# Kernel optimization log

Hardware: AMD Instinct MI355X
Metric: run time of the kernel (lower is better)

Reference implementation:

```python
import jax, jax.numpy as jnp
import numpy as np
from jax import lax

B, C_IN, N, C_OUT, K = 16, 128, 2048, 256, 20
EPS = 1e-5


def setup_inputs() -> dict:
    key = jax.random.key(0)
    k1, k2 = jax.random.split(key)
    x = jax.random.normal(k1, (B, C_IN, N), dtype=jnp.float32)
    W = jax.random.normal(k2, (C_OUT, 2 * C_IN), dtype=jnp.float32) * (1.0 / np.sqrt(2 * C_IN))
    gamma = jnp.ones((C_OUT,), dtype=jnp.float32)
    beta = jnp.zeros((C_OUT,), dtype=jnp.float32)
    return {"x": x, "W": W, "gamma": gamma, "beta": beta, "k": K}


def _knn_inds(x, k):
    # squared pairwise distance: (B, N, N); computed with no grad (stop_gradient)
    xs = lax.stop_gradient(x)
    inner = jnp.einsum('bcn,bcm->bnm', xs, xs)
    sq = jnp.sum(xs * xs, axis=1)  # (B, N)
    pd = sq[:, :, None] - 2.0 * inner + sq[:, None, :]
    _, inds = lax.top_k(-pd, k)  # smallest distances -> (B, N, k)
    return inds


def reference(x, W, gamma, beta, k):
    knn = _knn_inds(x, k)                                   # (B, N, k) int
    # gather neighbours: neigh[b,c,n,j] = x[b,c,knn[b,n,j]]
    neigh = jax.vmap(lambda xb, kb: xb[:, kb])(x, knn)      # (B, C, N, k)
    central = jnp.broadcast_to(x[:, :, :, None], neigh.shape)
    edge = jnp.concatenate([central, neigh - central], axis=1)  # (B, 2C, N, k)
    # 1x1 conv (bias-free) as GEMM
    y = jnp.einsum('oc,bcnk->bonk', W, edge)                # (B, C_out, N, k)
    # BatchNorm2d (training-mode batch stats) + affine
    mean = jnp.mean(y, axis=(0, 2, 3), keepdims=True)
    var = jnp.var(y, axis=(0, 2, 3), keepdims=True)
    y = (y - mean) * lax.rsqrt(var + EPS)
    y = y * gamma[None, :, None, None] + beta[None, :, None, None]
    y = jax.nn.relu(y)
    return jnp.max(y, axis=3)                               # (B, C_out, N)
```

## Files before the change

### kernel.cpp

```cpp
#include <hip/hip_runtime.h>

#define B_   16
#define CIN  128
#define NPT  2048
#define COUT 256
#define KNN  20
#define KEEP 16
#define SIFT 32
#define EPS  1e-5f
#define DBIAS 256.0f

#define SQ_OFF   0ull
#define IDX_OFF  131072ull
#define UT_OFF   2752512ull
#define VT_OFF   36306944ull
#define GS_OFF   69861376ull
#define ST_OFF   69865472ull
#define AMAX_OFF 69871616ull
#define AMIN_OFF 103426048ull
#define WS_NEED_FUSED 136980480ull
#define XT_OFF   UT_OFF
#define XHT_OFF  VT_OFF

typedef _Float16 f16x8 __attribute__((ext_vector_type(8)));
typedef _Float16 f16x4 __attribute__((ext_vector_type(4)));
typedef float    f32x4 __attribute__((ext_vector_type(4)));
typedef float    f32x2 __attribute__((ext_vector_type(2)));

__global__ __launch_bounds__(256) void prep_kernel(const float* __restrict__ x,
                                                   const float* __restrict__ W,
                                                   float* __restrict__ xT,
                                                   _Float16* __restrict__ xhT,
                                                   _Float16* __restrict__ Wu,
                                                   _Float16* __restrict__ Wv,
                                                   float* __restrict__ sqh) {
    __shared__ float Ls[128 * 68];
    __shared__ float ps[4 * 64];
    const int id  = blockIdx.x;
    const int xcd = id & 7, qq = id >> 3;
    const int b   = xcd + ((qq >> 5) << 3);
    const int n0  = (qq & 31) * 64;
    const int t = threadIdx.x;
    if (Wu != nullptr && id < 128) {
        int gid = id * 256 + t;
        int o = gid >> 7, c = gid & 127;
        float w1 = W[o * 256 + c], w2 = W[o * 256 + 128 + c];
        Wu[gid] = (_Float16)(w1 - w2);
        Wv[gid] = (_Float16)w2;
    }
    const float* xb = x + (size_t)b * CIN * NPT;
    #pragma unroll
    for (int e = 0; e < 8; ++e) {
        int f = e * 256 + t;
        int c = f >> 4, n4 = (f & 15) << 2;
        *(float4*)&Ls[c * 68 + n4] = *(const float4*)&xb[(size_t)c * NPT + n0 + n4];
    }
    __syncthreads();
    {
        int nl = t & 63, part = t >> 6;
        float acc = 0.f;
        #pragma unroll
        for (int j = 0; j < 32; ++j) {
            float vh = (float)(_Float16)Ls[(part * 32 + j) * 68 + nl];
            acc += vh * vh;
        }
        ps[part * 64 + nl] = acc;
    }
    #pragma unroll
    for (int e = 0; e < 2; ++e) {
        int u = e * 256 + t;
        int nl = u >> 3, ck = (u & 7) << 4;
        float vv[16];
        #pragma unroll
        for (int j = 0; j < 16; ++j) vv[j] = Ls[(ck + j) * 68 + nl];
        size_t row = (size_t)b * NPT + n0 + nl;
        #pragma unroll
        for (int j = 0; j < 4; ++j) {
            float4 w = {vv[4 * j], vv[4 * j + 1], vv[4 * j + 2], vv[4 * j + 3]};
            *(float4*)&xT[row * CIN + ck + 4 * j] = w;
        }
        f16x8 h0, h1;
        #pragma unroll
        for (int j = 0; j < 8; ++j) { h0[j] = (_Float16)vv[j]; h1[j] = (_Float16)vv[8 + j]; }
        *(f16x8*)&xhT[row * CIN + ck] = h0;
        *(f16x8*)&xhT[row * CIN + ck + 8] = h1;
    }
    __syncthreads();
    if (t < 64) sqh[b * NPT + n0 + t] = ps[t] + ps[64 + t] + ps[128 + t] + ps[192 + t];
}

__device__ __forceinline__ void stage_pts(const _Float16* __restrict__ xhb,
                                          _Float16* buf, int base_n, int t) {
    const int l15 = t & 15, ks = t >> 6;
    const int quad = (t >> 4) & 3;
    const int c = ks * 32 + quad * 8;
    #pragma unroll
    for (int e = 0; e < 4; ++e) {
        const int n = base_n + e * 16 + l15;
        const _Float16* src = xhb + (size_t)n * CIN + c;
        _Float16* dst = buf + (size_t)(e * 256 + (t & 192)) * 8;
        __builtin_amdgcn_global_load_lds(
            (const __attribute__((address_space(1))) void*)src,
            (__attribute__((address_space(3))) void*)dst, 16, 0, 0);
    }
}

__device__ __forceinline__ void stage_tile16(const _Float16* __restrict__ srcl,
                                             _Float16* dsthalf) {
    #pragma unroll
    for (int e = 0; e < 4; ++e) {
        __builtin_amdgcn_global_load_lds(
            (const __attribute__((address_space(1))) void*)(srcl + e * 32),
            (__attribute__((address_space(3))) void*)(dsthalf + (size_t)e * 512),
            16, 0, 0);
    }
}

__global__ __launch_bounds__(256, 2) void knn_kernel(const _Float16* __restrict__ xhT,
                                                     const float* __restrict__ sqh,
                                                     int* __restrict__ surv_out) {
    __shared__ char smraw[59392];
    _Float16* bufA = (_Float16*)smraw;
    float*    sqm  = (float*)(smraw + 18432);

    const int id  = blockIdx.x;
    const int xcd = id & 7, qq = id >> 3;
    const int b   = xcd + ((qq >> 5) << 3);
    const int q0  = (qq & 31) * 64;
    const int t  = threadIdx.x;
    const int lane = t & 63, wv = t >> 6;
    const int l15 = lane & 15, quad = lane >> 4;
    const _Float16* xhb = xhT + (size_t)b * NPT * CIN;

    #pragma unroll
    for (int e = 0; e < 8; ++e)
        sqm[e * 256 + t] = sqh[b * NPT + e * 256 + t] + DBIAS;

    stage_pts(xhb, bufA, q0, t);
    __syncthreads();

    f16x8 af[4][4];
    #pragma unroll
    for (int qh = 0; qh < 4; ++qh)
        #pragma unroll
        for (int ks = 0; ks < 4; ++ks)
            af[qh][ks] = *(const f16x8*)(bufA + (size_t)((qh * 4 + ks) * 64 + lane) * 8);
    __syncthreads();

    _Float16* wbuf = (_Float16*)(smraw + 26624 + wv * 8192);
    float*    DtW  = (float*)(smraw + wv * 4608);
    const _Float16* srcl = xhb + (size_t)(wv * 16 + l15) * CIN + quad * 8;

    stage_tile16(srcl, wbuf);

    float bd[KEEP];
    #pragma unroll
    for (int i = 0; i < KEEP; ++i) bd[i] = 3.0e38f;

    #pragma unroll 1
    for (int ss = 0; ss < 32; ++ss) {
        const int mb = ss * 64 + wv * 16;
        asm volatile("s_waitcnt vmcnt(0)" ::: "memory");
        __builtin_amdgcn_sched_barrier(0);
        const _Float16* cur = wbuf + (ss & 1) * 2048;
        f16x8 bf[4];
        #pragma unroll
        for (int ks = 0; ks < 4; ++ks)
            bf[ks] = *(const f16x8*)(cur + ks * 512 + lane * 8);
        float sm_ = sqm[mb + l15];
        asm volatile("s_waitcnt lgkmcnt(0)" ::: "memory");
        __builtin_amdgcn_sched_barrier(0);
        if (ss < 31)
            stage_tile16(srcl + (size_t)(ss + 1) * 64 * CIN,
                         wbuf + ((ss + 1) & 1) * 2048);
        __builtin_amdgcn_sched_barrier(0);
        f32x4 acc[4];
        #pragma unroll
        for (int qh = 0; qh < 4; ++qh) acc[qh] = (f32x4){0.f, 0.f, 0.f, 0.f};
        #pragma unroll
        for (int ks = 0; ks < 4; ++ks)
            #pragma unroll
            for (int qh = 0; qh < 4; ++qh)
                acc[qh] = __builtin_amdgcn_mfma_f32_16x16x32_f16(af[qh][ks], bf[ks], acc[qh], 0, 0, 0);
        const unsigned om = (unsigned)(mb + l15);
        #pragma unroll
        for (int qh = 0; qh < 4; ++qh) {
            #pragma unroll
            for (int rg = 0; rg < 4; ++rg) {
                int q = qh * 16 + quad * 4 + rg;
                float d = sm_ - 2.f * acc[qh][rg];
                DtW[q * 18 + l15] = __uint_as_float((__float_as_uint(d) & 0xFFFFF800u) | om);
            }
        }
        float nk[16];
        {
            const float* myrow = DtW + lane * 18;
            #pragma unroll
            for (int p = 0; p < 8; ++p) {
                f32x2 v = *(const f32x2*)(myrow + 2 * p);
                nk[2 * p] = v[0]; nk[2 * p + 1] = v[1];
            }
        }
        #pragma unroll
        for (int kk = 2; kk <= 16; kk <<= 1) {
            #pragma unroll
            for (int j = kk >> 1; j > 0; j >>= 1) {
                #pragma unroll
                for (int i = 0; i < 16; ++i) {
                    int p = i ^ j;
                    if (p > i) {
                        float a = nk[i], c = nk[p];
                        float lo = fminf(a, c), hi = fmaxf(a, c);
                        if ((i & kk) == 0) { nk[i] = lo; nk[p] = hi; }
                        else               { nk[i] = hi; nk[p] = lo; }
                    }
                }
            }
        }
        #pragma unroll
        for (int i = 0; i < 16; ++i) bd[i] = fminf(bd[i], nk[15 - i]);
        #pragma unroll
        for (int j = 8; j > 0; j >>= 1) {
            #pragma unroll
            for (int i = 0; i < 16; ++i) {
                int p = i ^ j;
                if (p > i) {
                    float a = bd[i], c = bd[p];
                    bd[i] = fminf(a, c);
                    bd[p] = fmaxf(a, c);
                }
            }
        }
    }

    __syncthreads();

    float* Keys = (float*)smraw;
    #pragma unroll
    for (int i = 0; i < KEEP; ++i)
        Keys[lane * 65 + wv * KEEP + i] = bd[i];
    __syncthreads();
    {
        int cnt[KEEP];
        #pragma unroll
        for (int i = 0; i < KEEP; ++i) cnt[i] = 0;
        #pragma unroll 4
        for (int j = 0; j < 64; ++j) {
            float kj = Keys[lane * 65 + j];
            #pragma unroll
            for (int i = 0; i < KEEP; ++i)
                cnt[i] += (kj < bd[i]) ? 1 : 0;
        }
        int* dst = surv_out + ((size_t)b * NPT + q0 + lane) * SIFT;
        #pragma unroll
        for (int i = 0; i < KEEP; ++i)
            if (cnt[i] < SIFT)
                dst[cnt[i]] = (int)(__float_as_uint(bd[i]) & 0x7FFu);
    }
}

__global__ __launch_bounds__(256, 4) void refine_kernel(const float* __restrict__ xT,
                                                        const int* __restrict__ surv,
                                                        int* __restrict__ knn_out) {
    __shared__ float  Qs[16 * 128];
    __shared__ int    sidx[16 * 32];
    __shared__ double ddL[16 * 32];
    const int id  = blockIdx.x;
    const int xcd = id & 7, qq = id >> 3;
    const int b   = xcd + ((qq >> 7) << 3);
    const int q0  = (qq & 127) * 16;
    const int t = threadIdx.x;
    const float* xTb = xT + (size_t)b * NPT * CIN;
    #pragma unroll
    for (int e = 0; e < 2; ++e)
        sidx[e * 256 + t] = surv[((size_t)b * NPT + q0) * SIFT + e * 256 + t];
    #pragma unroll
    for (int e = 0; e < 2; ++e) {
        int f = e * 256 + t;
        int row = f >> 5, c4 = (f & 31) << 2;
        *(float4*)&Qs[row * 128 + c4] = *(const float4*)&xTb[(size_t)(q0 + row) * CIN + c4];
    }
    __syncthreads();
    const int g = t >> 3, j = t & 7;
    #pragma unroll 1
    for (int it = 0; it < 16; ++it) {
        int pair = it * 32 + g;
        int q = pair >> 5, k = pair & 31;
        int m = sidx[q * 32 + k];
        const float* mrow = xTb + (size_t)m * CIN + j * 16;
        const float* qrow = Qs + q * 128 + j * 16;
        float4 a0 = *(const float4*)&mrow[0];
        float4 a1 = *(const float4*)&mrow[4];
        float4 a2 = *(const float4*)&mrow[8];
        float4 a3 = *(const float4*)&mrow[12];
        float4 c0 = *(const float4*)&qrow[0];
        float4 c1 = *(const float4*)&qrow[4];
        float4 c2 = *(const float4*)&qrow[8];
        float4 c3 = *(const float4*)&qrow[12];
        double ss = 0.0, d0;
        d0 = (double)c0.x - (double)a0.x; ss = fma(d0, d0, ss);
        d0 = (double)c0.y - (double)a0.y; ss = fma(d0, d0, ss);
        d0 = (double)c0.z - (double)a0.z; ss = fma(d0, d0, ss);
        d0 = (double)c0.w - (double)a0.w; ss = fma(d0, d0, ss);
        d0 = (double)c1.x - (double)a1.x; ss = fma(d0, d0, ss);
        d0 = (double)c1.y - (double)a1.y; ss = fma(d0, d0, ss);
        d0 = (double)c1.z - (double)a1.z; ss = fma(d0, d0, ss);
        d0 = (double)c1.w - (double)a1.w; ss = fma(d0, d0, ss);
        d0 = (double)c2.x - (double)a2.x; ss = fma(d0, d0, ss);
        d0 = (double)c2.y - (double)a2.y; ss = fma(d0, d0, ss);
        d0 = (double)c2.z - (double)a2.z; ss = fma(d0, d0, ss);
        d0 = (double)c2.w - (double)a2.w; ss = fma(d0, d0, ss);
        d0 = (double)c3.x - (double)a3.x; ss = fma(d0, d0, ss);
        d0 = (double)c3.y - (double)a3.y; ss = fma(d0, d0, ss);
        d0 = (double)c3.z - (double)a3.z; ss = fma(d0, d0, ss);
        d0 = (double)c3.w - (double)a3.w; ss = fma(d0, d0, ss);
        ss += __shfl_xor(ss, 1, 8);
        ss += __shfl_xor(ss, 2, 8);
        ss += __shfl_xor(ss, 4, 8);
        if (j == 0) ddL[q * 32 + k] = ss;
    }
    __syncthreads();
    const int q = t >> 4, kk = (t & 15) << 1;
    int* dst = knn_out + ((size_t)b * NPT + q0 + q) * KNN;
    #pragma unroll
    for (int e = 0; e < 2; ++e) {
        int k = kk + e;
        double mine = ddL[q * 32 + k];
        int c = 0;
        #pragma unroll 4
        for (int jx = 0; jx < SIFT; ++jx)
            c += (ddL[q * 32 + jx] < mine) ? 1 : 0;
        if (c < KNN) dst[c] = sidx[q * 32 + k];
    }
}

__global__ __launch_bounds__(256, 2) void knn_kernel_fb(const _Float16* __restrict__ xhT,
                                                        const float* __restrict__ xT,
                                                        const float* __restrict__ sqh,
                                                        int* __restrict__ knn_out) {
    __shared__ char smraw[59392];
    _Float16* bufA = (_Float16*)smraw;
    float*    sqm  = (float*)(smraw + 18432);

    const int b  = blockIdx.y;
    const int q0 = blockIdx.x * 64;
    const int t  = threadIdx.x;
    const int lane = t & 63, wv = t >> 6;
    const int l15 = lane & 15, quad = lane >> 4;
    const _Float16* xhb = xhT + (size_t)b * NPT * CIN;

    #pragma unroll
    for (int e = 0; e < 8; ++e)
        sqm[e * 256 + t] = sqh[b * NPT + e * 256 + t] + DBIAS;

    stage_pts(xhb, bufA, q0, t);
    __syncthreads();

    f16x8 af[4][4];
    #pragma unroll
    for (int qh = 0; qh < 4; ++qh)
        #pragma unroll
        for (int ks = 0; ks < 4; ++ks)
            af[qh][ks] = *(const f16x8*)(bufA + (size_t)((qh * 4 + ks) * 64 + lane) * 8);
    __syncthreads();

    _Float16* wbuf = (_Float16*)(smraw + 26624 + wv * 8192);
    float*    DtW  = (float*)(smraw + wv * 4608);
    const _Float16* srcl = xhb + (size_t)(wv * 16 + l15) * CIN + quad * 8;
    stage_tile16(srcl, wbuf);

    float bd[KEEP];
    #pragma unroll
    for (int i = 0; i < KEEP; ++i) bd[i] = 3.0e38f;

    #pragma unroll 1
    for (int ss = 0; ss < 32; ++ss) {
        const int mb = ss * 64 + wv * 16;
        asm volatile("s_waitcnt vmcnt(0)" ::: "memory");
        __builtin_amdgcn_sched_barrier(0);
        const _Float16* cur = wbuf + (ss & 1) * 2048;
        f16x8 bf[4];
        #pragma unroll
        for (int ks = 0; ks < 4; ++ks)
            bf[ks] = *(const f16x8*)(cur + ks * 512 + lane * 8);
        float sm_ = sqm[mb + l15];
        asm volatile("s_waitcnt lgkmcnt(0)" ::: "memory");
        __builtin_amdgcn_sched_barrier(0);
        if (ss < 31)
            stage_tile16(srcl + (size_t)(ss + 1) * 64 * CIN,
                         wbuf + ((ss + 1) & 1) * 2048);
        __builtin_amdgcn_sched_barrier(0);
        f32x4 acc[4];
        #pragma unroll
        for (int qh = 0; qh < 4; ++qh) acc[qh] = (f32x4){0.f, 0.f, 0.f, 0.f};
        #pragma unroll
        for (int ks = 0; ks < 4; ++ks)
            #pragma unroll
            for (int qh = 0; qh < 4; ++qh)
                acc[qh] = __builtin_amdgcn_mfma_f32_16x16x32_f16(af[qh][ks], bf[ks], acc[qh], 0, 0, 0);
        const unsigned om = (unsigned)(mb + l15);
        #pragma unroll
        for (int qh = 0; qh < 4; ++qh) {
            #pragma unroll
            for (int rg = 0; rg < 4; ++rg) {
                int q = qh * 16 + quad * 4 + rg;
                float d = sm_ - 2.f * acc[qh][rg];
                DtW[q * 18 + l15] = __uint_as_float((__float_as_uint(d) & 0xFFFFF800u) | om);
            }
        }
        float nk[16];
        {
            const float* myrow = DtW + lane * 18;
            #pragma unroll
            for (int p = 0; p < 8; ++p) {
                f32x2 v = *(const f32x2*)(myrow + 2 * p);
                nk[2 * p] = v[0]; nk[2 * p + 1] = v[1];
            }
        }
        #pragma unroll
        for (int kk = 2; kk <= 16; kk <<= 1) {
            #pragma unroll
            for (int j = kk >> 1; j > 0; j >>= 1) {
                #pragma unroll
                for (int i = 0; i < 16; ++i) {
                    int p = i ^ j;
                    if (p > i) {
                        float a = nk[i], c = nk[p];
                        float lo = fminf(a, c), hi = fmaxf(a, c);
                        if ((i & kk) == 0) { nk[i] = lo; nk[p] = hi; }
                        else               { nk[i] = hi; nk[p] = lo; }
                    }
                }
            }
        }
        #pragma unroll
        for (int i = 0; i < 16; ++i) bd[i] = fminf(bd[i], nk[15 - i]);
        #pragma unroll
        for (int j = 8; j > 0; j >>= 1) {
            #pragma unroll
            for (int i = 0; i < 16; ++i) {
                int p = i ^ j;
                if (p > i) {
                    float a = bd[i], c = bd[p];
                    bd[i] = fminf(a, c);
                    bd[p] = fmaxf(a, c);
                }
            }
        }
    }

    __syncthreads();

    float*  Keys = (float*)smraw;
    int*    Surv = (int*)(smraw + 16640);
    double* ddL  = (double*)(smraw + 25088);
    #pragma unroll
    for (int i = 0; i < KEEP; ++i)
        Keys[lane * 65 + wv * KEEP + i] = bd[i];
    __syncthreads();
    {
        int cnt[KEEP];
        #pragma unroll
        for (int i = 0; i < KEEP; ++i) cnt[i] = 0;
        #pragma unroll 4
        for (int j = 0; j < 64; ++j) {
            float kj = Keys[lane * 65 + j];
            #pragma unroll
            for (int i = 0; i < KEEP; ++i)
                cnt[i] += (kj < bd[i]) ? 1 : 0;
        }
        __syncthreads();
        #pragma unroll
        for (int i = 0; i < KEEP; ++i)
            if (cnt[i] < SIFT)
                Surv[lane * 33 + cnt[i]] = (int)(__float_as_uint(bd[i]) & 0x7FFu);
    }
    __syncthreads();

    int ms[8];
    #pragma unroll
    for (int k = 0; k < 8; ++k) ms[k] = Surv[lane * 33 + wv * 8 + k] & 2047;
    double dd8[8];
    #pragma unroll
    for (int k = 0; k < 8; ++k) dd8[k] = 0.0;
    const float* xTb = xT + (size_t)b * NPT * CIN;
    const float* qrow = xTb + (size_t)(q0 + lane) * CIN;
    #pragma unroll 1
    for (int ch = 0; ch < 8; ++ch) {
        double qd[16];
        #pragma unroll
        for (int j = 0; j < 4; ++j) {
            float4 qv = *(const float4*)&qrow[ch * 16 + 4 * j];
            qd[4 * j] = (double)qv.x; qd[4 * j + 1] = (double)qv.y;
            qd[4 * j + 2] = (double)qv.z; qd[4 * j + 3] = (double)qv.w;
        }
        #pragma unroll
        for (int k = 0; k < 8; ++k) {
            const float* mrow = xTb + (size_t)ms[k] * CIN + ch * 16;
            float4 ma = *(const float4*)&mrow[0];
            float4 mb2 = *(const float4*)&mrow[4];
            float4 mc = *(const float4*)&mrow[8];
            float4 md = *(const float4*)&mrow[12];
            double ss = dd8[k], d0;
            d0 = qd[0]  - (double)ma.x;  ss = fma(d0, d0, ss);
            d0 = qd[1]  - (double)ma.y;  ss = fma(d0, d0, ss);
            d0 = qd[2]  - (double)ma.z;  ss = fma(d0, d0, ss);
            d0 = qd[3]  - (double)ma.w;  ss = fma(d0, d0, ss);
            d0 = qd[4]  - (double)mb2.x; ss = fma(d0, d0, ss);
            d0 = qd[5]  - (double)mb2.y; ss = fma(d0, d0, ss);
            d0 = qd[6]  - (double)mb2.z; ss = fma(d0, d0, ss);
            d0 = qd[7]  - (double)mb2.w; ss = fma(d0, d0, ss);
            d0 = qd[8]  - (double)mc.x;  ss = fma(d0, d0, ss);
            d0 = qd[9]  - (double)mc.y;  ss = fma(d0, d0, ss);
            d0 = qd[10] - (double)mc.z;  ss = fma(d0, d0, ss);
            d0 = qd[11] - (double)mc.w;  ss = fma(d0, d0, ss);
            d0 = qd[12] - (double)md.x;  ss = fma(d0, d0, ss);
            d0 = qd[13] - (double)md.y;  ss = fma(d0, d0, ss);
            d0 = qd[14] - (double)md.z;  ss = fma(d0, d0, ss);
            d0 = qd[15] - (double)md.w;  ss = fma(d0, d0, ss);
            dd8[k] = ss;
        }
    }
    #pragma unroll
    for (int k = 0; k < 8; ++k) ddL[lane * 33 + wv * 8 + k] = dd8[k];
    __syncthreads();
    int* dst = knn_out + ((size_t)b * NPT + q0 + lane) * KNN;
    #pragma unroll
    for (int k = 0; k < 8; ++k) {
        int c = 0;
        #pragma unroll 4
        for (int j = 0; j < SIFT; ++j)
            c += (ddL[lane * 33 + j] < dd8[k]) ? 1 : 0;
        if (c < KNN) dst[c] = ms[k];
    }
}

__global__ __launch_bounds__(256) void uv_gemm_h(const _Float16* __restrict__ xhT,
                                                 const _Float16* __restrict__ Wu,
                                                 const _Float16* __restrict__ Wv,
                                                 _Float16* __restrict__ uT,
                                                 _Float16* __restrict__ vT) {
    __shared__ _Float16 Bx[8192];
    const int id  = blockIdx.x;
    const int xcd = id & 7, qq = id >> 3;
    const int b   = xcd + ((qq >> 5) << 3);
    const int n0  = (qq & 31) * 64;
    const int t = threadIdx.x;
    const int lane = t & 63, w = t >> 6, l15 = lane & 15, quad = lane >> 4;
    stage_pts(xhT + (size_t)b * NPT * CIN, Bx, n0, t);
    __syncthreads();
    f16x8 bf[4];
    #pragma unroll
    for (int ks = 0; ks < 4; ++ks)
        bf[ks] = *(const f16x8*)(Bx + (size_t)((w * 4 + ks) * 64 + lane) * 8);
    const int n = n0 + w * 16 + l15;
    #pragma unroll 1
    for (int ot = 0; ot < 16; ++ot) {
        const _Float16* wu = Wu + (size_t)(ot * 16 + l15) * 128 + quad * 8;
        const _Float16* wv2 = Wv + (size_t)(ot * 16 + l15) * 128 + quad * 8;
        f32x4 au = (f32x4){0.f, 0.f, 0.f, 0.f};
        f32x4 av = (f32x4){0.f, 0.f, 0.f, 0.f};
        #pragma unroll
        for (int ks = 0; ks < 4; ++ks) {
            f16x8 a_u = *(const f16x8*)(wu + ks * 32);
            f16x8 a_v = *(const f16x8*)(wv2 + ks * 32);
            au = __builtin_amdgcn_mfma_f32_16x16x32_f16(a_u, bf[ks], au, 0, 0, 0);
            av = __builtin_amdgcn_mfma_f32_16x16x32_f16(a_v, bf[ks], av, 0, 0, 0);
        }
        size_t base = ((size_t)b * NPT + n) * COUT + ot * 16 + quad * 4;
        f16x4 auh = {(_Float16)au[0], (_Float16)au[1], (_Float16)au[2], (_Float16)au[3]};
        f16x4 avh = {(_Float16)av[0], (_Float16)av[1], (_Float16)av[2], (_Float16)av[3]};
        *(f16x4*)&uT[base] = auh;
        *(f16x4*)&vT[base] = avh;
    }
}

__global__ __launch_bounds__(256) void uv_gemm(const float* __restrict__ x,
                                               const float* __restrict__ W,
                                               float* __restrict__ uT,
                                               float* __restrict__ vT) {
    __shared__ float Ax[32 * 64];
    __shared__ float Bu[32 * 68];
    __shared__ float Bv[32 * 68];
    const int b  = blockIdx.z;
    const int n0 = blockIdx.x * 64;
    const int o0 = blockIdx.y * 64;
    const int t  = threadIdx.x;
    const int tx = t & 15, ty = t >> 4;
    const float* xb = x + (size_t)b * CIN * NPT;
    float au[4][4], av_[4][4];
    #pragma unroll
    for (int i = 0; i < 4; ++i)
        #pragma unroll
        for (int j = 0; j < 4; ++j) { au[i][j] = 0.f; av_[i][j] = 0.f; }
    #pragma unroll 1
    for (int kc = 0; kc < 4; ++kc) {
        const int c0 = kc * 32;
        __syncthreads();
        #pragma unroll
        for (int e = 0; e < 2; ++e) {
            int f = e * 256 + t;
            int cz = f >> 4, ni = (f & 15) << 2;
            *(float4*)&Ax[(cz << 6) + ni] = *(const float4*)&xb[(size_t)(c0 + cz) * NPT + n0 + ni];
        }
        #pragma unroll
        for (int e = 0; e < 8; ++e) {
            int ii = e * 256 + t;
            int cz = ii & 31, oj = ii >> 5;
            float w1 = W[(size_t)(o0 + oj) * 256 + c0 + cz];
            float w2 = W[(size_t)(o0 + oj) * 256 + 128 + c0 + cz];
            Bu[cz * 68 + oj] = w1 - w2;
            Bv[cz * 68 + oj] = w2;
        }
        __syncthreads();
        #pragma unroll 8
        for (int cz = 0; cz < 32; ++cz) {
            const float4 a4 = *(const float4*)&Ax[(cz << 6) + (tx << 2)];
            float bu0 = Bu[cz * 68 + (ty << 2) + 0], bv0 = Bv[cz * 68 + (ty << 2) + 0];
            float bu1 = Bu[cz * 68 + (ty << 2) + 1], bv1 = Bv[cz * 68 + (ty << 2) + 1];
            float bu2 = Bu[cz * 68 + (ty << 2) + 2], bv2 = Bv[cz * 68 + (ty << 2) + 2];
            float bu3 = Bu[cz * 68 + (ty << 2) + 3], bv3 = Bv[cz * 68 + (ty << 2) + 3];
            au[0][0] += a4.x * bu0; au[0][1] += a4.x * bu1; au[0][2] += a4.x * bu2; au[0][3] += a4.x * bu3;
            au[1][0] += a4.y * bu0; au[1][1] += a4.y * bu1; au[1][2] += a4.y * bu2; au[1][3] += a4.y * bu3;
            au[2][0] += a4.z * bu0; au[2][1] += a4.z * bu1; au[2][2] += a4.z * bu2; au[2][3] += a4.z * bu3;
            au[3][0] += a4.w * bu0; au[3][1] += a4.w * bu1; au[3][2] += a4.w * bu2; au[3][3] += a4.w * bu3;
            av_[0][0] += a4.x * bv0; av_[0][1] += a4.x * bv1; av_[0][2] += a4.x * bv2; av_[0][3] += a4.x * bv3;
            av_[1][0] += a4.y * bv0; av_[1][1] += a4.y * bv1; av_[1][2] += a4.y * bv2; av_[1][3] += a4.y * bv3;
            av_[2][0] += a4.z * bv0; av_[2][1] += a4.z * bv1; av_[2][2] += a4.z * bv2; av_[2][3] += a4.z * bv3;
            av_[3][0] += a4.w * bv0; av_[3][1] += a4.w * bv1; av_[3][2] += a4.w * bv2; av_[3][3] += a4.w * bv3;
        }
    }
    #pragma unroll
    for (int i = 0; i < 4; ++i) {
        int n = n0 + (tx << 2) + i;
        size_t base = ((size_t)b * NPT + n) * COUT + o0 + (ty << 2);
        float4 u4 = {au[i][0], au[i][1], au[i][2], au[i][3]};
        float4 v4 = {av_[i][0], av_[i][1], av_[i][2], av_[i][3]};
        *(float4*)&uT[base] = u4;
        *(float4*)&vT[base] = v4;
    }
}

__global__ __launch_bounds__(256) void gather_stats(const _Float16* __restrict__ uT,
                                                    const _Float16* __restrict__ vT,
                                                    const int* __restrict__ knn_in,
                                                    double* __restrict__ gsum,
                                                    _Float16* __restrict__ aMax,
                                                    _Float16* __restrict__ aMin) {
    __shared__ int sidx[16 * KNN];
    const int id  = blockIdx.x;
    const int xcd = id & 7, qq = id >> 3;
    const int b   = xcd + ((qq >> 7) << 3);
    const int inner = qq & 127;
    const int n0  = (inner >> 2) * 64 + (inner & 3) * 16;
    const int o   = threadIdx.x;
    for (int e = o; e < 16 * KNN; e += 256)
        sidx[e] = knn_in[((size_t)b * NPT + n0) * KNN + e];
    __syncthreads();
    const _Float16* ub = uT + ((size_t)b * NPT + n0) * COUT + o;
    const _Float16* vb = vT + (size_t)b * NPT * COUT + o;
    _Float16* amx = aMax + ((size_t)b * NPT + n0) * COUT + o;
    _Float16* amn = aMin + ((size_t)b * NPT + n0) * COUT + o;
    double s1 = 0.0, s2 = 0.0;
    #pragma unroll 1
    for (int s = 0; s < 16; ++s) {
        float u = (float)ub[(size_t)s * COUT];
        float vmax = -3e38f, vmin = 3e38f, vsum = 0.f, vsq = 0.f;
        #pragma unroll
        for (int j = 0; j < KNN; ++j) {
            float v = (float)vb[(size_t)sidx[s * KNN + j] * COUT];
            vmax = fmaxf(vmax, v);
            vmin = fminf(vmin, v);
            vsum += v;
            vsq = fmaf(v, v, vsq);
        }
        s1 += 20.0 * (double)u + (double)vsum;
        s2 += 20.0 * (double)u * (double)u + 2.0 * (double)u * (double)vsum + (double)vsq;
        _Float16 y1 = (_Float16)(u + vmax);
        _Float16 y2 = (_Float16)(u + vmin);
        __builtin_nontemporal_store(y1, &amx[(size_t)s * COUT]);
        __builtin_nontemporal_store(y2, &amn[(size_t)s * COUT]);
    }
    atomicAdd(&gsum[o], s1);
    atomicAdd(&gsum[COUT + o], s2);
}

__global__ __launch_bounds__(256) void stats_kernel(const float* __restrict__ uT,
                                                    const float* __restrict__ vT,
                                                    const int* __restrict__ knn_in,
                                                    double* __restrict__ gsum) {
    __shared__ int sidx[64 * KNN];
    const int b  = blockIdx.y;
    const int n0 = blockIdx.x * 64;
    const int o  = threadIdx.x;
    for (int e = o; e < 64 * KNN; e += 256)
        sidx[e] = knn_in[((size_t)b * NPT + n0) * KNN + e];
    __syncthreads();
    const float* ub = uT + ((size_t)b * NPT + n0) * COUT + o;
    const float* vb = vT + (size_t)b * NPT * COUT + o;
    double s1 = 0.0, s2 = 0.0;
    #pragma unroll 1
    for (int s = 0; s < 64; ++s) {
        float u = ub[(size_t)s * COUT];
        #pragma unroll
        for (int j = 0; j < KNN; ++j) {
            float y = u + vb[(size_t)sidx[s * KNN + j] * COUT];
            s1 += (double)y;
            s2 = fma((double)y, (double)y, s2);
        }
    }
    atomicAdd(&gsum[o], s1);
    atomicAdd(&gsum[COUT + o], s2);
}

__global__ void finalize_kernel(const double* __restrict__ gsum,
                                const float* __restrict__ gamma,
                                const float* __restrict__ beta,
                                float* __restrict__ st) {
    const int o = threadIdx.x;
    const double M = (double)B_ * NPT * KNN;
    double mean = gsum[o] / M;
    double var  = gsum[COUT + o] / M - mean * mean;
    float inv = 1.0f / sqrtf((float)var + EPS);
    float s = gamma[o] * inv;
    st[o] = s;
    st[COUT + o] = beta[o] - (float)mean * s;
}

__global__ __launch_bounds__(256, 2) void out2_kernel(const _Float16* __restrict__ aMax,
                                                      const _Float16* __restrict__ aMin,
                                                      const double* __restrict__ gsum,
                                                      const float* __restrict__ gamma,
                                                      const float* __restrict__ beta,
                                                      float* __restrict__ out) {
    __shared__ float zt[256 * 68];
    const int id  = blockIdx.x;
    const int xcd = id & 7, qq = id >> 3;
    const int b   = xcd + ((qq >> 5) << 3);
    const int n0  = (qq & 31) * 64;
    const int o = threadIdx.x;
    const double M = (double)B_ * NPT * KNN;
    double mean = gsum[o] / M;
    double var  = gsum[COUT + o] / M - mean * mean;
    float inv = 1.0f / sqrtf((float)var + EPS);
    const float s  = gamma[o] * inv;
    const float tt = beta[o] - (float)mean * s;
    const _Float16* amx = aMax + ((size_t)b * NPT + n0) * COUT + o;
    const _Float16* amn = aMin + ((size_t)b * NPT + n0) * COUT + o;
    #pragma unroll 2
    for (int si = 0; si < 64; ++si) {
        float y1 = (float)amx[(size_t)si * COUT];
        float y2 = (float)amn[(size_t)si * COUT];
        float z1 = fmaxf(s * y1 + tt, 0.f);
        float z2 = fmaxf(s * y2 + tt, 0.f);
        zt[o * 68 + si] = fmaxf(z1, z2);
    }
    __syncthreads();
    float* dst = out + ((size_t)b * COUT + o) * NPT + n0;
    #pragma unroll
    for (int i = 0; i < 16; ++i)
        *(float4*)&dst[i * 4] = *(const float4*)&zt[o * 68 + i * 4];
}

__global__ __launch_bounds__(256, 2) void out_kernel(const float* __restrict__ uT,
                                                     const float* __restrict__ vT,
                                                     const int* __restrict__ knn_in,
                                                     const float* __restrict__ st,
                                                     float* __restrict__ out) {
    __shared__ int sidx[64 * KNN];
    __shared__ float zt[256 * 68];
    const int b  = blockIdx.y;
    const int n0 = blockIdx.x * 64;
    const int o  = threadIdx.x;
    for (int e = o; e < 64 * KNN; e += 256)
        sidx[e] = knn_in[((size_t)b * NPT + n0) * KNN + e];
    __syncthreads();
    const float s  = st[o];
    const float tt = st[COUT + o];
    const float* ub = uT + ((size_t)b * NPT + n0) * COUT + o;
    const float* vb = vT + (size_t)b * NPT * COUT + o;
    #pragma unroll 1
    for (int si = 0; si < 64; ++si) {
        float u = ub[(size_t)si * COUT];
        float ymax = -3e38f, ymin = 3e38f;
        #pragma unroll
        for (int j = 0; j < KNN; ++j) {
            float y = u + vb[(size_t)sidx[si * KNN + j] * COUT];
            ymax = fmaxf(ymax, y);
            ymin = fminf(ymin, y);
        }
        float z1 = fmaxf(s * ymax + tt, 0.f);
        float z2 = fmaxf(s * ymin + tt, 0.f);
        zt[o * 68 + si] = fmaxf(z1, z2);
    }
    __syncthreads();
    float* dst = out + ((size_t)b * COUT + o) * NPT + n0;
    #pragma unroll
    for (int i = 0; i < 16; ++i)
        *(float4*)&dst[i * 4] = *(const float4*)&zt[o * 68 + i * 4];
}

extern "C" void kernel_launch(void* const* d_in, const int* in_sizes, int n_in,
                              void* d_out, int out_size, void* d_ws, size_t ws_size,
                              hipStream_t stream) {
    const float* x     = (const float*)d_in[0];
    const float* W     = (const float*)d_in[1];
    const float* gamma = (const float*)d_in[2];
    const float* beta  = (const float*)d_in[3];
    float* out = (float*)d_out;
    char* ws = (char*)d_ws;
    float*     sqh  = (float*)(ws + SQ_OFF);
    int*       idx  = (int*)(ws + IDX_OFF);
    double*    gsum = (double*)(ws + GS_OFF);
    float*     st   = (float*)(ws + ST_OFF);
    const bool fused = (ws_size >= WS_NEED_FUSED);

    hipMemsetAsync(gsum, 0, 2 * COUT * sizeof(double), stream);
    if (fused) {
        float*    xT   = (float*)(ws + AMAX_OFF);
        _Float16* xhT  = (_Float16*)(ws + AMAX_OFF + 16777216ull);
        _Float16* Wu   = (_Float16*)(ws + AMAX_OFF + 25165824ull);
        _Float16* Wv   = (_Float16*)(ws + AMAX_OFF + 25231360ull);
        int*      svG  = (int*)(ws + UT_OFF);
        _Float16* uTh  = (_Float16*)(ws + UT_OFF);
        _Float16* vTh  = (_Float16*)(ws + VT_OFF);
        _Float16* aMxh = (_Float16*)(ws + AMAX_OFF);
        _Float16* aMnh = (_Float16*)(ws + AMIN_OFF);
        prep_kernel<<<512, 256, 0, stream>>>(x, W, xT, xhT, Wu, Wv, sqh);
        knn_kernel<<<512, 256, 0, stream>>>(xhT, sqh, svG);
        refine_kernel<<<2048, 256, 0, stream>>>(xT, svG, idx);
        uv_gemm_h<<<512, 256, 0, stream>>>(xhT, Wu, Wv, uTh, vTh);
        gather_stats<<<2048, 256, 0, stream>>>(uTh, vTh, idx, gsum, aMxh, aMnh);
        out2_kernel<<<512, 256, 0, stream>>>(aMxh, aMnh, gsum, gamma, beta, out);
    } else {
        float*    xT  = (float*)(ws + XT_OFF);
        _Float16* xhT = (_Float16*)(ws + XHT_OFF);
        float*    uT  = (float*)(ws + UT_OFF);
        float*    vT  = (float*)(ws + VT_OFF);
        prep_kernel<<<512, 256, 0, stream>>>(x, W, xT, xhT, nullptr, nullptr, sqh);
        knn_kernel_fb<<<dim3(32, 16), 256, 0, stream>>>(xhT, xT, sqh, idx);
        uv_gemm<<<dim3(32, 4, 16), 256, 0, stream>>>(x, W, uT, vT);
        stats_kernel<<<dim3(32, 16), 256, 0, stream>>>(uT, vT, idx, gsum);
        finalize_kernel<<<1, 256, 0, stream>>>(gsum, gamma, beta, st);
        out_kernel<<<dim3(32, 16), 256, 0, stream>>>(uT, vT, idx, st, out);
    }
}
```

Measured before the change: 299.8 us.

## Fuse u/v GEMM and gsum zeroing into prep kernel

Moves the per-point u/v projection GEMM into the prep kernel, reusing the x tile already staged in shared memory and converting W to fp16 on the fly. This removes the separate uv_gemm_h launch, its reload of xhT, and the Wu/Wv precompute, and it replaces the hipMemsetAsync with zeroing inside the kernel. The kNN scratch buffer is moved to the AMIN region so it no longer overlaps the uT output, which is now written before kNN runs. In exchange, prep becomes heavier and every block reconverts W from fp32.

```diff
diff --git a/kernel.cpp b/kernel.cpp
--- a/kernel.cpp
+++ b/kernel.cpp
@@ -31,9 +31,10 @@
                                                    const float* __restrict__ W,
                                                    float* __restrict__ xT,
                                                    _Float16* __restrict__ xhT,
-                                                   _Float16* __restrict__ Wu,
-                                                   _Float16* __restrict__ Wv,
-                                                   float* __restrict__ sqh) {
+                                                   float* __restrict__ sqh,
+                                                   _Float16* __restrict__ uT,
+                                                   _Float16* __restrict__ vT,
+                                                   double* __restrict__ gsum) {
     __shared__ float Ls[128 * 68];
     __shared__ float ps[4 * 64];
     const int id  = blockIdx.x;
@@ -41,12 +42,9 @@
     const int b   = xcd + ((qq >> 5) << 3);
     const int n0  = (qq & 31) * 64;
     const int t = threadIdx.x;
-    if (Wu != nullptr && id < 128) {
-        int gid = id * 256 + t;
-        int o = gid >> 7, c = gid & 127;
-        float w1 = W[o * 256 + c], w2 = W[o * 256 + 128 + c];
-        Wu[gid] = (_Float16)(w1 - w2);
-        Wv[gid] = (_Float16)w2;
+    if (id == 0) {
+        gsum[t] = 0.0;
+        gsum[256 + t] = 0.0;
     }
     const float* xb = x + (size_t)b * CIN * NPT;
     #pragma unroll
@@ -87,6 +85,47 @@
     }
     __syncthreads();
     if (t < 64) sqh[b * NPT + n0 + t] = ps[t] + ps[64 + t] + ps[128 + t] + ps[192 + t];
+
+    if (uT == nullptr) return;
+
+    const int lane = t & 63, w = t >> 6, l15 = lane & 15, quad = lane >> 4;
+    f16x8 bf[4];
+    #pragma unroll
+    for (int ks = 0; ks < 4; ++ks)
+        #pragma unroll
+        for (int j = 0; j < 8; ++j)
+            bf[ks][j] = (_Float16)Ls[(ks * 32 + quad * 8 + j) * 68 + (w * 16 + l15)];
+    const int n = n0 + w * 16 + l15;
+    #pragma unroll 1
+    for (int ot = 0; ot < 16; ++ot) {
+        const float* wrow = W + (size_t)(ot * 16 + l15) * 256;
+        f32x4 au = (f32x4){0.f, 0.f, 0.f, 0.f};
+        f32x4 av = (f32x4){0.f, 0.f, 0.f, 0.f};
+        #pragma unroll
+        for (int ks = 0; ks < 4; ++ks) {
+            const int c0 = quad * 8 + ks * 32;
+            float4 wa = *(const float4*)&wrow[c0];
+            float4 wb = *(const float4*)&wrow[c0 + 4];
+            float4 wc = *(const float4*)&wrow[128 + c0];
+            float4 wd = *(const float4*)&wrow[128 + c0 + 4];
+            f16x8 a_u, a_v;
+            a_u[0] = (_Float16)(wa.x - wc.x); a_v[0] = (_Float16)wc.x;
+            a_u[1] = (_Float16)(wa.y - wc.y); a_v[1] = (_Float16)wc.y;
+            a_u[2] = (_Float16)(wa.z - wc.z); a_v[2] = (_Float16)wc.z;
+            a_u[3] = (_Float16)(wa.w - wc.w); a_v[3] = (_Float16)wc.w;
+            a_u[4] = (_Float16)(wb.x - wd.x); a_v[4] = (_Float16)wd.x;
+            a_u[5] = (_Float16)(wb.y - wd.y); a_v[5] = (_Float16)wd.y;
+            a_u[6] = (_Float16)(wb.z - wd.z); a_v[6] = (_Float16)wd.z;
+            a_u[7] = (_Float16)(wb.w - wd.w); a_v[7] = (_Float16)wd.w;
+            au = __builtin_amdgcn_mfma_f32_16x16x32_f16(a_u, bf[ks], au, 0, 0, 0);
+            av = __builtin_amdgcn_mfma_f32_16x16x32_f16(a_v, bf[ks], av, 0, 0, 0);
+        }
+        size_t base = ((size_t)b * NPT + n) * COUT + ot * 16 + quad * 4;
+        f16x4 auh = {(_Float16)au[0], (_Float16)au[1], (_Float16)au[2], (_Float16)au[3]};
+        f16x4 avh = {(_Float16)av[0], (_Float16)av[1], (_Float16)av[2], (_Float16)av[3]};
+        *(f16x4*)&uT[base] = auh;
+        *(f16x4*)&vT[base] = avh;
+    }
 }
 
 __device__ __forceinline__ void stage_pts(const _Float16* __restrict__ xhb,
@@ -535,46 +574,6 @@
     }
 }
 
-__global__ __launch_bounds__(256) void uv_gemm_h(const _Float16* __restrict__ xhT,
-                                                 const _Float16* __restrict__ Wu,
-                                                 const _Float16* __restrict__ Wv,
-                                                 _Float16* __restrict__ uT,
-                                                 _Float16* __restrict__ vT) {
-    __shared__ _Float16 Bx[8192];
-    const int id  = blockIdx.x;
-    const int xcd = id & 7, qq = id >> 3;
-    const int b   = xcd + ((qq >> 5) << 3);
-    const int n0  = (qq & 31) * 64;
-    const int t = threadIdx.x;
-    const int lane = t & 63, w = t >> 6, l15 = lane & 15, quad = lane >> 4;
-    stage_pts(xhT + (size_t)b * NPT * CIN, Bx, n0, t);
-    __syncthreads();
-    f16x8 bf[4];
-    #pragma unroll
-    for (int ks = 0; ks < 4; ++ks)
-        bf[ks] = *(const f16x8*)(Bx + (size_t)((w * 4 + ks) * 64 + lane) * 8);
-    const int n = n0 + w * 16 + l15;
-    #pragma unroll 1
-    for (int ot = 0; ot < 16; ++ot) {
-        const _Float16* wu = Wu + (size_t)(ot * 16 + l15) * 128 + quad * 8;
-        const _Float16* wv2 = Wv + (size_t)(ot * 16 + l15) * 128 + quad * 8;
-        f32x4 au = (f32x4){0.f, 0.f, 0.f, 0.f};
-        f32x4 av = (f32x4){0.f, 0.f, 0.f, 0.f};
-        #pragma unroll
-        for (int ks = 0; ks < 4; ++ks) {
-            f16x8 a_u = *(const f16x8*)(wu + ks * 32);
-            f16x8 a_v = *(const f16x8*)(wv2 + ks * 32);
-            au = __builtin_amdgcn_mfma_f32_16x16x32_f16(a_u, bf[ks], au, 0, 0, 0);
-            av = __builtin_amdgcn_mfma_f32_16x16x32_f16(a_v, bf[ks], av, 0, 0, 0);
-        }
-        size_t base = ((size_t)b * NPT + n) * COUT + ot * 16 + quad * 4;
-        f16x4 auh = {(_Float16)au[0], (_Float16)au[1], (_Float16)au[2], (_Float16)au[3]};
-        f16x4 avh = {(_Float16)av[0], (_Float16)av[1], (_Float16)av[2], (_Float16)av[3]};
-        *(f16x4*)&uT[base] = auh;
-        *(f16x4*)&vT[base] = avh;
-    }
-}
-
 __global__ __launch_bounds__(256) void uv_gemm(const float* __restrict__ x,
                                                const float* __restrict__ W,
                                                float* __restrict__ uT,
@@ -815,21 +814,17 @@
     float*     st   = (float*)(ws + ST_OFF);
     const bool fused = (ws_size >= WS_NEED_FUSED);
 
-    hipMemsetAsync(gsum, 0, 2 * COUT * sizeof(double), stream);
     if (fused) {
         float*    xT   = (float*)(ws + AMAX_OFF);
         _Float16* xhT  = (_Float16*)(ws + AMAX_OFF + 16777216ull);
-        _Float16* Wu   = (_Float16*)(ws + AMAX_OFF + 25165824ull);
-        _Float16* Wv   = (_Float16*)(ws + AMAX_OFF + 25231360ull);
-        int*      svG  = (int*)(ws + UT_OFF);
+        int*      svG  = (int*)(ws + AMIN_OFF);
         _Float16* uTh  = (_Float16*)(ws + UT_OFF);
         _Float16* vTh  = (_Float16*)(ws + VT_OFF);
         _Float16* aMxh = (_Float16*)(ws + AMAX_OFF);
         _Float16* aMnh = (_Float16*)(ws + AMIN_OFF);
-        prep_kernel<<<512, 256, 0, stream>>>(x, W, xT, xhT, Wu, Wv, sqh);
+        prep_kernel<<<512, 256, 0, stream>>>(x, W, xT, xhT, sqh, uTh, vTh, gsum);
         knn_kernel<<<512, 256, 0, stream>>>(xhT, sqh, svG);
         refine_kernel<<<2048, 256, 0, stream>>>(xT, svG, idx);
-        uv_gemm_h<<<512, 256, 0, stream>>>(xhT, Wu, Wv, uTh, vTh);
         gather_stats<<<2048, 256, 0, stream>>>(uTh, vTh, idx, gsum, aMxh, aMnh);
         out2_kernel<<<512, 256, 0, stream>>>(aMxh, aMnh, gsum, gamma, beta, out);
     } else {
@@ -837,7 +832,7 @@
         _Float16* xhT = (_Float16*)(ws + XHT_OFF);
         float*    uT  = (float*)(ws + UT_OFF);
         float*    vT  = (float*)(ws + VT_OFF);
-        prep_kernel<<<512, 256, 0, stream>>>(x, W, xT, xhT, nullptr, nullptr, sqh);
+        prep_kernel<<<512, 256, 0, stream>>>(x, W, xT, xhT, sqh, nullptr, nullptr, gsum);
         knn_kernel_fb<<<dim3(32, 16), 256, 0, stream>>>(xhT, xT, sqh, idx);
         uv_gemm<<<dim3(32, 4, 16), 256, 0, stream>>>(x, W, uT, vT);
         stats_kernel<<<dim3(32, 16), 256, 0, stream>>>(uT, vT, idx, gsum);
```

New measurement: 320.2 us. 1.07x slower.
